# Kernel optimization log

Measured on AMD Instinct MI355X. Metric: run time of the kernel, lower is better.

Reference implementation:

```python
import jax, jax.numpy as jnp
import numpy as np

N, E, F, H, C = 50000, 800000, 128, 128, 64
NEG_SLOPE = 0.2


def setup_inputs() -> dict:
    key = jax.random.key(0)
    ks = jax.random.split(key, 12)
    s = 1.0 / np.sqrt(H)
    return {
        "x": jax.random.normal(ks[0], (N, F), jnp.float32),
        "edge_index": jax.random.randint(ks[1], (2, E), 0, N, jnp.int64),
        "W1": jax.random.normal(ks[2], (F, H), jnp.float32) * s,
        "b1": jnp.zeros((H,), jnp.float32),
        "Wg1": jax.random.normal(ks[3], (H, H), jnp.float32) * s,
        "asrc1": jax.random.normal(ks[4], (H,), jnp.float32) * s,
        "adst1": jax.random.normal(ks[5], (H,), jnp.float32) * s,
        "bg1": jnp.zeros((H,), jnp.float32),
        "W2": jax.random.normal(ks[6], (H, H), jnp.float32) * s,
        "b2": jnp.zeros((H,), jnp.float32),
        "Wg2": jax.random.normal(ks[7], (H, H), jnp.float32) * s,
        "asrc2": jax.random.normal(ks[8], (H,), jnp.float32) * s,
        "adst2": jax.random.normal(ks[9], (H,), jnp.float32) * s,
        "bg2": jnp.zeros((H,), jnp.float32),
        "Wo": jax.random.normal(ks[10], (H, C), jnp.float32) * s,
        "bo": jnp.zeros((C,), jnp.float32),
    }


def _gcn(x, src, dst, n, W, b):
    # PyG GCNConv: add self-loops (done by caller), symmetric normalization
    xw = x @ W
    deg = jax.ops.segment_sum(jnp.ones(src.shape[0], xw.dtype), dst, num_segments=n)
    inv = jax.lax.rsqrt(deg)  # deg >= 1 due to self-loops
    coef = inv[src] * inv[dst]
    return jax.ops.segment_sum(coef[:, None] * xw[src], dst, num_segments=n) + b


def _gat(x, src, dst, n, W, a_s, a_d, b):
    # PyG GATConv, heads=1: segment softmax over destination nodes
    xw = x @ W
    e = jax.nn.leaky_relu((xw @ a_s)[src] + (xw @ a_d)[dst], NEG_SLOPE)
    m = jax.ops.segment_max(e, dst, num_segments=n)
    ex = jnp.exp(e - m[dst])
    denom = jax.ops.segment_sum(ex, dst, num_segments=n)
    alpha = ex / denom[dst]
    return jax.ops.segment_sum(alpha[:, None] * xw[src], dst, num_segments=n) + b


def reference(x, edge_index, W1, b1, Wg1, asrc1, adst1, bg1,
              W2, b2, Wg2, asrc2, adst2, bg2, Wo, bo):
    n = x.shape[0]
    loops = jnp.arange(n, dtype=edge_index.dtype)
    src = jnp.concatenate([edge_index[0], loops])
    dst = jnp.concatenate([edge_index[1], loops])

    h = jax.nn.relu(_gcn(x, src, dst, n, W1, b1))
    h = jax.nn.relu(_gat(h, src, dst, n, Wg1, asrc1, adst1, bg1))
    h = jax.nn.relu(_gcn(h, src, dst, n, W2, b2))
    h = jax.nn.relu(_gat(h, src, dst, n, Wg2, asrc2, adst2, bg2))
    z = h @ Wo + bo
    return (h, z)
```

## Files before the change

kernel.cpp:

```cpp
#include <hip/hip_runtime.h>
#include <hip/hip_bf16.h>
#include <hip/hip_fp16.h>


#define WAVE 64
#define BK 256
#define CHUNK 4096

typedef _Float16 f16x8 __attribute__((ext_vector_type(8)));
typedef float f32x4 __attribute__((ext_vector_type(4)));

__global__ void k_zero_i32(int* __restrict__ p, int n) {
    int i = blockIdx.x * 256 + threadIdx.x;
    if (i < n) p[i] = 0;
}


__global__ __launch_bounds__(256) void k_bhist(
    const int* __restrict__ ei, int* __restrict__ bcnt,
    int E, int Et, int nbuck) {
    __shared__ int hist[256];
    int tid = threadIdx.x;
    if (tid < nbuck) hist[tid] = 0;
    __syncthreads();
    for (int e = blockIdx.x * 256 + tid; e < Et; e += gridDim.x * 256) {
        int d = (e < E) ? ei[E + e] : (e - E);
        atomicAdd(&hist[d >> 8], 1);
    }
    __syncthreads();
    if (tid < nbuck && hist[tid] > 0) atomicAdd(&bcnt[tid], hist[tid]);
}

__global__ void k_bscan(const int* __restrict__ bcnt, int* __restrict__ bbase,
                        int* __restrict__ bcur, int nbuck) {
    __shared__ int tmp[256];
    int tid = threadIdx.x;
    int v = (tid < nbuck) ? bcnt[tid] : 0;
    tmp[tid] = v;
    __syncthreads();
    for (int off = 1; off < 256; off <<= 1) {
        int t = (tid >= off) ? tmp[tid - off] : 0;
        __syncthreads();
        tmp[tid] += t;
        __syncthreads();
    }
    if (tid < nbuck) {
        int excl = tmp[tid] - v;
        bbase[tid] = excl;
        bcur[tid] = excl;
        if (tid == nbuck - 1) bbase[nbuck] = tmp[tid];
    }
}

__global__ __launch_bounds__(256) void k_bscatter(
    const int* __restrict__ ei, int* __restrict__ bcur,
    int2* __restrict__ ebuf, int E, int Et, int nbuck) {
    __shared__ int hist[256];
    __shared__ int base[256];
    __shared__ int off[256];
    constexpr int PT = CHUNK / 256;
    int tid = threadIdx.x;
    int cb = blockIdx.x * CHUNK;
    if (tid < nbuck) { hist[tid] = 0; off[tid] = 0; }
    __syncthreads();

    int sv[PT], dv[PT];
#pragma unroll
    for (int i = 0; i < PT; ++i) {
        int e = cb + i * 256 + tid;
        int s = 0, d = -1;
        if (e < Et) {
            if (e < E) { s = ei[e]; d = ei[E + e]; }
            else       { s = d = e - E; }
            atomicAdd(&hist[d >> 8], 1);
        }
        sv[i] = s; dv[i] = d;
    }
    __syncthreads();
    if (tid < nbuck && hist[tid] > 0)
        base[tid] = atomicAdd(&bcur[tid], hist[tid]);
    __syncthreads();
#pragma unroll
    for (int i = 0; i < PT; ++i) {
        if (dv[i] >= 0) {
            int b = dv[i] >> 8;
            int pos = base[b] + atomicAdd(&off[b], 1);
            ebuf[pos] = make_int2(sv[i], dv[i]);
        }
    }
}

__global__ __launch_bounds__(256) void k_csr(
    const int2* __restrict__ ebuf, const int* __restrict__ bbase,
    int* __restrict__ rowp, float* __restrict__ inv, int* __restrict__ esrc,
    int Nn, int Et) {
    __shared__ int hist[256];
    __shared__ int scan[256];
    __shared__ int cur[256];
    int tid = threadIdx.x;
    int b = blockIdx.x;
    int bb = bbase[b], cnt = bbase[b + 1] - bb;
    hist[tid] = 0;
    __syncthreads();
    for (int t = tid; t < cnt; t += 256)
        atomicAdd(&hist[ebuf[bb + t].y & 255], 1);
    __syncthreads();
    int v = hist[tid];
    scan[tid] = v;
    __syncthreads();
    for (int o = 1; o < 256; o <<= 1) {
        int t = (tid >= o) ? scan[tid - o] : 0;
        __syncthreads();
        scan[tid] += t;
        __syncthreads();
    }
    int excl = scan[tid] - v;
    int node = b * BK + tid;
    if (node < Nn) {
        rowp[node] = bb + excl;
        inv[node] = rsqrtf((float)v);
    }
    cur[tid] = excl;
    if (b == 0 && tid == 0) rowp[Nn] = Et;
    __syncthreads();
    for (int t = tid; t < cnt; t += 256) {
        int2 e = ebuf[bb + t];
        int pos = bb + atomicAdd(&cur[e.y & 255], 1);
        esrc[pos] = e.x;
    }
}


__global__ void k_wcvt(const float* __restrict__ W1, const float* __restrict__ Wg1,
                       const float* __restrict__ W2, const float* __restrict__ Wg2,
                       const float* __restrict__ Wo, __half* __restrict__ Wt) {
    int i = blockIdx.x * 256 + threadIdx.x;
    if (i < 65536) {
        int w = i >> 14;
        int j = i & 16383;
        int nt = j >> 11, ks = (j >> 9) & 3, lane = (j >> 3) & 63, jj = j & 7;
        int n = nt * 16 + (lane & 15);
        int k = ks * 32 + (lane >> 4) * 8 + jj;
        const float* W = (w == 0) ? W1 : (w == 1) ? Wg1 : (w == 2) ? W2 : Wg2;
        Wt[i] = __float2half(W[k * 128 + n]);
    } else if (i < 73728) {
        int j = i - 65536;
        int nt = j >> 11, ks = (j >> 9) & 3, lane = (j >> 3) & 63, jj = j & 7;
        int n = nt * 16 + (lane & 15);
        int k = ks * 32 + (lane >> 4) * 8 + jj;
        Wt[65536 + j] = __float2half(Wo[k * 64 + n]);
    }
}


template <int NC, typename OT>
__global__ __launch_bounds__(256) void gemm_mfma(
    const float* __restrict__ A, const __half* __restrict__ Wt,
    const float* __restrict__ bias, OT* __restrict__ out,
    const float* __restrict__ asrc, const float* __restrict__ adst,
    float* __restrict__ alS, float* __restrict__ alD, int M) {
    constexpr int NT = NC / 16;
    __shared__ f16x8 Wl[NC * 16];
    const int tid = threadIdx.x;
    const int wv = tid >> 6, lane = tid & 63;
    const int m16 = lane & 15, quad = lane >> 4;

#pragma unroll
    for (int i = tid; i < NC * 16; i += 256)
        Wl[i] = ((const f16x8*)Wt)[i];
    __syncthreads();

    const int row0 = blockIdx.x * 64 + wv * 16;

    f16x8 af[4];
    {
        int row = row0 + m16;
        if (row > M - 1) row = M - 1;
        const float* ap = A + (size_t)row * 128 + quad * 8;
#pragma unroll
        for (int ks = 0; ks < 4; ++ks) {
            float4 lo = *(const float4*)(ap + ks * 32);
            float4 hi = *(const float4*)(ap + ks * 32 + 4);
            f16x8 v;
            v[0] = (_Float16)lo.x; v[1] = (_Float16)lo.y;
            v[2] = (_Float16)lo.z; v[3] = (_Float16)lo.w;
            v[4] = (_Float16)hi.x; v[5] = (_Float16)hi.y;
            v[6] = (_Float16)hi.z; v[7] = (_Float16)hi.w;
            af[ks] = v;
        }
    }

    f32x4 acc[NT];
#pragma unroll
    for (int nt = 0; nt < NT; ++nt)
        acc[nt] = (f32x4){0.f, 0.f, 0.f, 0.f};

#pragma unroll
    for (int ks = 0; ks < 4; ++ks) {
#pragma unroll
        for (int nt = 0; nt < NT; ++nt) {
            f16x8 bf = Wl[(nt * 4 + ks) * 64 + lane];
            acc[nt] = __builtin_amdgcn_mfma_f32_16x16x32_f16(
                af[ks], bf, acc[nt], 0, 0, 0);
        }
    }

    if (asrc) {
        float sa[NT], da[NT];
#pragma unroll
        for (int nt = 0; nt < NT; ++nt) {
            sa[nt] = asrc[nt * 16 + m16];
            da[nt] = adst[nt * 16 + m16];
        }
#pragma unroll
        for (int r = 0; r < 4; ++r) {
            float s = 0.f, d = 0.f;
#pragma unroll
            for (int nt = 0; nt < NT; ++nt) {
                s = fmaf(acc[nt][r], sa[nt], s);
                d = fmaf(acc[nt][r], da[nt], d);
            }
#pragma unroll
            for (int off = 8; off > 0; off >>= 1) {
                s += __shfl_xor(s, off);
                d += __shfl_xor(d, off);
            }
            int row = row0 + quad * 4 + r;
            if (m16 == 0 && row < M) { alS[row] = s; alD[row] = d; }
        }
    }

#pragma unroll
    for (int nt = 0; nt < NT; ++nt) {
#pragma unroll
        for (int r = 0; r < 4; ++r) {
            int row = row0 + quad * 4 + r;
            if (row < M) {
                float v = acc[nt][r];
                int col = nt * 16 + m16;
                if constexpr (sizeof(OT) == 2) {
                    ((__half*)out)[(size_t)row * NC + col] = __float2half(v);
                } else {
                    ((float*)out)[(size_t)row * NC + col] = v + bias[col];
                }
            }
        }
    }
}


__device__ __forceinline__ void gather_accum_h(
    const __half* __restrict__ xw, int q, int g, int cnt, int sid, float wgt,
    float acc[8]) {
    for (int base = 0; base < cnt; base += 32) {
        int c = cnt - base;
        float4 x[8];
        float w[8];
#pragma unroll
        for (int u = 0; u < 8; ++u) {
            if (u * 4 < c) {
                int idx = base + 4 * u + g;
                int s = __shfl(sid, idx);
                w[u] = __shfl(wgt, idx);
                x[u] = *(const float4*)(xw + (size_t)s * 128 + q * 8);
            }
        }
#pragma unroll
        for (int u = 0; u < 8; ++u) {
            if (u * 4 < c) {
                const __half2* h2 = (const __half2*)&x[u];
#pragma unroll
                for (int i = 0; i < 4; ++i) {
                    float2 cc = __half22float2(h2[i]);
                    acc[2 * i]     = fmaf(w[u], cc.x, acc[2 * i]);
                    acc[2 * i + 1] = fmaf(w[u], cc.y, acc[2 * i + 1]);
                }
            }
        }
    }
}

__device__ __forceinline__ void finish_store_q(
    float acc[8], const float* __restrict__ bias, float* __restrict__ out,
    int n, int q, int g) {
#pragma unroll
    for (int i = 0; i < 8; ++i) {
        acc[i] += __shfl_xor(acc[i], 16);
        acc[i] += __shfl_xor(acc[i], 32);
    }
    if (g == 0) {
        float4 b0 = ((const float4*)bias)[q * 2];
        float4 b1 = ((const float4*)bias)[q * 2 + 1];
        float4 r0, r1;
        r0.x = fmaxf(acc[0] + b0.x, 0.f);
        r0.y = fmaxf(acc[1] + b0.y, 0.f);
        r0.z = fmaxf(acc[2] + b0.z, 0.f);
        r0.w = fmaxf(acc[3] + b0.w, 0.f);
        r1.x = fmaxf(acc[4] + b1.x, 0.f);
        r1.y = fmaxf(acc[5] + b1.y, 0.f);
        r1.z = fmaxf(acc[6] + b1.z, 0.f);
        r1.w = fmaxf(acc[7] + b1.w, 0.f);
        float4* orow = (float4*)(out + (size_t)n * 128);
        orow[q * 2]     = r0;
        orow[q * 2 + 1] = r1;
    }
}

__global__ __launch_bounds__(256) void k_gcn_agg(
    const __half* __restrict__ xw, const int* __restrict__ rowp,
    const int* __restrict__ esrc, const float* __restrict__ inv,
    const float* __restrict__ bias, float* __restrict__ out, int Nn) {
    int gid = blockIdx.x * 256 + threadIdx.x;
    int n = gid >> 6, lane = gid & 63;
    if (n >= Nn) return;
    int q = lane & 15, g = lane >> 4;
    int beg = rowp[n], end = rowp[n + 1];
    float invd = inv[n];
    float acc[8] = {0.f, 0.f, 0.f, 0.f, 0.f, 0.f, 0.f, 0.f};
    for (int base = beg; base < end; base += WAVE) {
        int e = base + lane;
        bool valid = (e < end);
        int sid = valid ? esrc[e] : 0;
        float c = valid ? invd * inv[sid] : 0.f;
        gather_accum_h(xw, q, g, min(WAVE, end - base), sid, c, acc);
    }
    finish_store_q(acc, bias, out, n, q, g);
}

__global__ __launch_bounds__(256) void k_gat_agg(
    const __half* __restrict__ xw, const int* __restrict__ rowp,
    const int* __restrict__ esrc, const float* __restrict__ as_,
    const float* __restrict__ ad_, const float* __restrict__ bias,
    float* __restrict__ out, int Nn) {
    int gid = blockIdx.x * 256 + threadIdx.x;
    int n = gid >> 6, lane = gid & 63;
    if (n >= Nn) return;
    int q = lane & 15, g = lane >> 4;
    int beg = rowp[n], end = rowp[n + 1];
    int deg = end - beg;
    float adn = ad_[n];
    float acc[8] = {0.f, 0.f, 0.f, 0.f, 0.f, 0.f, 0.f, 0.f};

    if (deg <= WAVE) {
        bool valid = (lane < deg);
        int sid = 0;
        float v = -1e30f;
        if (valid) {
            sid = esrc[beg + lane];
            float t = as_[sid] + adn;
            v = (t > 0.f) ? t : 0.2f * t;
        }
        float m = v;
#pragma unroll
        for (int off = 32; off > 0; off >>= 1) m = fmaxf(m, __shfl_xor(m, off));
        float ex = valid ? __expf(v - m) : 0.f;
        float ssum = ex;
#pragma unroll
        for (int off = 32; off > 0; off >>= 1) ssum += __shfl_xor(ssum, off);
        float wgt = ex * (1.f / ssum);
        gather_accum_h(xw, q, g, deg, sid, wgt, acc);
    } else {
        float m = -1e30f, ssum = 0.f;
        for (int e = beg + lane; e < end; e += WAVE) {
            float v = as_[esrc[e]] + adn;
            v = (v > 0.f) ? v : 0.2f * v;
            float mn = fmaxf(m, v);
            ssum = ssum * __expf(m - mn) + __expf(v - mn);
            m = mn;
        }
#pragma unroll
        for (int off = 32; off > 0; off >>= 1) {
            float mo = __shfl_xor(m, off);
            float so = __shfl_xor(ssum, off);
            float mn = fmaxf(m, mo);
            ssum = ssum * __expf(m - mn) + so * __expf(mo - mn);
            m = mn;
        }
        float rden = 1.f / ssum;
        for (int base = beg; base < end; base += WAVE) {
            int e = base + lane;
            bool valid = (e < end);
            int sid = valid ? esrc[e] : 0;
            float wgt = 0.f;
            if (valid) {
                float v = as_[sid] + adn;
                v = (v > 0.f) ? v : 0.2f * v;
                wgt = __expf(v - m) * rden;
            }
            gather_accum_h(xw, q, g, min(WAVE, end - base), sid, wgt, acc);
        }
    }
    finish_store_q(acc, bias, out, n, q, g);
}


extern "C" void kernel_launch(void* const* d_in, const int* in_sizes, int n_in,
                              void* d_out, int out_size, void* d_ws, size_t ws_size,
                              hipStream_t stream) {
    const float* x   = (const float*)d_in[0];
    const int*   ei  = (const int*)d_in[1];
    const float* W1  = (const float*)d_in[2];
    const float* b1  = (const float*)d_in[3];
    const float* Wg1 = (const float*)d_in[4];
    const float* as1 = (const float*)d_in[5];
    const float* ad1 = (const float*)d_in[6];
    const float* bg1 = (const float*)d_in[7];
    const float* W2  = (const float*)d_in[8];
    const float* b2  = (const float*)d_in[9];
    const float* Wg2 = (const float*)d_in[10];
    const float* as2 = (const float*)d_in[11];
    const float* ad2 = (const float*)d_in[12];
    const float* bg2 = (const float*)d_in[13];
    const float* Wo  = (const float*)d_in[14];
    const float* bo  = (const float*)d_in[15];

    const int Nn = in_sizes[0] / 128;
    const int E  = in_sizes[1] / 2;
    const int Et = E + Nn;
    const int H  = 128;
    const int nbuck = (Nn + BK - 1) / BK;

    float* outH = (float*)d_out;
    float* outZ = outH + (size_t)Nn * H;

    char* p = (char*)d_ws;
    auto carve = [&](size_t bytes) {
        char* r = p;
        p += (bytes + 255) & ~(size_t)255;
        return r;
    };
    __half* bufA = (__half*)carve((size_t)Nn * H * sizeof(__half));
    __half* Wt   = (__half*)carve((size_t)73728 * sizeof(__half));
    float* alS   = (float*)carve((size_t)Nn * sizeof(float));
    float* alD   = (float*)carve((size_t)Nn * sizeof(float));
    float* inv   = (float*)carve((size_t)Nn * sizeof(float));
    int*   rowp  = (int*)carve((size_t)(Nn + 1) * sizeof(int));
    int*   esrc  = (int*)carve((size_t)Et * sizeof(int));
    int2*  ebuf  = (int2*)carve((size_t)Et * sizeof(int2));
    int*   bcnt  = (int*)carve((size_t)nbuck * sizeof(int));
    int*   bbase = (int*)carve((size_t)(nbuck + 1) * sizeof(int));
    int*   bcur  = (int*)carve((size_t)nbuck * sizeof(int));
    (void)ws_size; (void)n_in; (void)out_size;

    const int aggBlocks = (Nn * WAVE + 255) / 256;
    const int gemmB = (Nn + 63) / 64;
    const int scatB = (Et + CHUNK - 1) / CHUNK;

    k_zero_i32<<<1, 256, 0, stream>>>(bcnt, nbuck);
    k_bhist<<<104, 256, 0, stream>>>(ei, bcnt, E, Et, nbuck);
    k_bscan<<<1, 256, 0, stream>>>(bcnt, bbase, bcur, nbuck);
    k_bscatter<<<scatB, 256, 0, stream>>>(ei, bcur, ebuf, E, Et, nbuck);
    k_csr<<<nbuck, 256, 0, stream>>>(ebuf, bbase, rowp, inv, esrc, Nn, Et);
    k_wcvt<<<288, 256, 0, stream>>>(W1, Wg1, W2, Wg2, Wo, Wt);

    gemm_mfma<128, __half><<<gemmB, 256, 0, stream>>>(
        x, Wt, nullptr, bufA, nullptr, nullptr, nullptr, nullptr, Nn);
    k_gcn_agg<<<aggBlocks, 256, 0, stream>>>(bufA, rowp, esrc, inv, b1, outH, Nn);

    gemm_mfma<128, __half><<<gemmB, 256, 0, stream>>>(
        outH, Wt + 16384, nullptr, bufA, as1, ad1, alS, alD, Nn);
    k_gat_agg<<<aggBlocks, 256, 0, stream>>>(bufA, rowp, esrc, alS, alD, bg1, outH, Nn);

    gemm_mfma<128, __half><<<gemmB, 256, 0, stream>>>(
        outH, Wt + 32768, nullptr, bufA, nullptr, nullptr, nullptr, nullptr, Nn);
    k_gcn_agg<<<aggBlocks, 256, 0, stream>>>(bufA, rowp, esrc, inv, b2, outH, Nn);

    gemm_mfma<128, __half><<<gemmB, 256, 0, stream>>>(
        outH, Wt + 49152, nullptr, bufA, as2, ad2, alS, alD, Nn);
    k_gat_agg<<<aggBlocks, 256, 0, stream>>>(bufA, rowp, esrc, alS, alD, bg2, outH, Nn);

    gemm_mfma<64, float><<<gemmB, 256, 0, stream>>>(
        outH, Wt + 65536, bo, outZ, nullptr, nullptr, nullptr, nullptr, Nn);
}
```

Before: 378.4 us.

## Slice feature layout and precompute per-edge weights for sliced aggregation

```diff
diff --git a/kernel.cpp b/kernel.cpp
--- a/kernel.cpp
+++ b/kernel.cpp
@@ -6,6 +6,7 @@
 #define WAVE 64
 #define BK 256
 #define CHUNK 4096
+#define NSLICE 4
 
 typedef _Float16 f16x8 __attribute__((ext_vector_type(8)));
 typedef float f32x4 __attribute__((ext_vector_type(4)));
@@ -239,7 +240,8 @@
                 float v = acc[nt][r];
                 int col = nt * 16 + m16;
                 if constexpr (sizeof(OT) == 2) {
-                    ((__half*)out)[(size_t)row * NC + col] = __float2half(v);
+                    size_t addr = ((size_t)(col >> 5) * M + row) * 32 + (col & 31);
+                    ((__half*)out)[addr] = __float2half(v);
                 } else {
                     ((float*)out)[(size_t)row * NC + col] = v + bias[col];
                 }
@@ -249,97 +251,30 @@
 }
 
 
-__device__ __forceinline__ void gather_accum_h(
-    const __half* __restrict__ xw, int q, int g, int cnt, int sid, float wgt,
-    float acc[8]) {
-    for (int base = 0; base < cnt; base += 32) {
-        int c = cnt - base;
-        float4 x[8];
-        float w[8];
-#pragma unroll
-        for (int u = 0; u < 8; ++u) {
-            if (u * 4 < c) {
-                int idx = base + 4 * u + g;
-                int s = __shfl(sid, idx);
-                w[u] = __shfl(wgt, idx);
-                x[u] = *(const float4*)(xw + (size_t)s * 128 + q * 8);
-            }
-        }
-#pragma unroll
-        for (int u = 0; u < 8; ++u) {
-            if (u * 4 < c) {
-                const __half2* h2 = (const __half2*)&x[u];
-#pragma unroll
-                for (int i = 0; i < 4; ++i) {
-                    float2 cc = __half22float2(h2[i]);
-                    acc[2 * i]     = fmaf(w[u], cc.x, acc[2 * i]);
-                    acc[2 * i + 1] = fmaf(w[u], cc.y, acc[2 * i + 1]);
-                }
-            }
-        }
-    }
-}
-
-__device__ __forceinline__ void finish_store_q(
-    float acc[8], const float* __restrict__ bias, float* __restrict__ out,
-    int n, int q, int g) {
-#pragma unroll
-    for (int i = 0; i < 8; ++i) {
-        acc[i] += __shfl_xor(acc[i], 16);
-        acc[i] += __shfl_xor(acc[i], 32);
-    }
-    if (g == 0) {
-        float4 b0 = ((const float4*)bias)[q * 2];
-        float4 b1 = ((const float4*)bias)[q * 2 + 1];
-        float4 r0, r1;
-        r0.x = fmaxf(acc[0] + b0.x, 0.f);
-        r0.y = fmaxf(acc[1] + b0.y, 0.f);
-        r0.z = fmaxf(acc[2] + b0.z, 0.f);
-        r0.w = fmaxf(acc[3] + b0.w, 0.f);
-        r1.x = fmaxf(acc[4] + b1.x, 0.f);
-        r1.y = fmaxf(acc[5] + b1.y, 0.f);
-        r1.z = fmaxf(acc[6] + b1.z, 0.f);
-        r1.w = fmaxf(acc[7] + b1.w, 0.f);
-        float4* orow = (float4*)(out + (size_t)n * 128);
-        orow[q * 2]     = r0;
-        orow[q * 2 + 1] = r1;
-    }
-}
-
-__global__ __launch_bounds__(256) void k_gcn_agg(
-    const __half* __restrict__ xw, const int* __restrict__ rowp,
-    const int* __restrict__ esrc, const float* __restrict__ inv,
-    const float* __restrict__ bias, float* __restrict__ out, int Nn) {
+__global__ __launch_bounds__(256) void k_wgcn(
+    const int* __restrict__ rowp, const int* __restrict__ esrc,
+    const float* __restrict__ inv, int2* __restrict__ ew, int Nn) {
     int gid = blockIdx.x * 256 + threadIdx.x;
     int n = gid >> 6, lane = gid & 63;
     if (n >= Nn) return;
-    int q = lane & 15, g = lane >> 4;
     int beg = rowp[n], end = rowp[n + 1];
     float invd = inv[n];
-    float acc[8] = {0.f, 0.f, 0.f, 0.f, 0.f, 0.f, 0.f, 0.f};
-    for (int base = beg; base < end; base += WAVE) {
-        int e = base + lane;
-        bool valid = (e < end);
-        int sid = valid ? esrc[e] : 0;
-        float c = valid ? invd * inv[sid] : 0.f;
-        gather_accum_h(xw, q, g, min(WAVE, end - base), sid, c, acc);
-    }
-    finish_store_q(acc, bias, out, n, q, g);
-}
-
-__global__ __launch_bounds__(256) void k_gat_agg(
-    const __half* __restrict__ xw, const int* __restrict__ rowp,
-    const int* __restrict__ esrc, const float* __restrict__ as_,
-    const float* __restrict__ ad_, const float* __restrict__ bias,
-    float* __restrict__ out, int Nn) {
+    for (int e = beg + lane; e < end; e += WAVE) {
+        int sid = esrc[e];
+        ew[e] = make_int2(sid, __float_as_int(invd * inv[sid]));
+    }
+}
+
+__global__ __launch_bounds__(256) void k_alpha(
+    const int* __restrict__ rowp, const int* __restrict__ esrc,
+    const float* __restrict__ as_, const float* __restrict__ ad_,
+    int2* __restrict__ ew, int Nn) {
     int gid = blockIdx.x * 256 + threadIdx.x;
     int n = gid >> 6, lane = gid & 63;
     if (n >= Nn) return;
-    int q = lane & 15, g = lane >> 4;
     int beg = rowp[n], end = rowp[n + 1];
     int deg = end - beg;
     float adn = ad_[n];
-    float acc[8] = {0.f, 0.f, 0.f, 0.f, 0.f, 0.f, 0.f, 0.f};
 
     if (deg <= WAVE) {
         bool valid = (lane < deg);
@@ -358,7 +293,7 @@
 #pragma unroll
         for (int off = 32; off > 0; off >>= 1) ssum += __shfl_xor(ssum, off);
         float wgt = ex * (1.f / ssum);
-        gather_accum_h(xw, q, g, deg, sid, wgt, acc);
+        if (valid) ew[beg + lane] = make_int2(sid, __float_as_int(wgt));
     } else {
         float m = -1e30f, ssum = 0.f;
         for (int e = beg + lane; e < end; e += WAVE) {
@@ -377,20 +312,74 @@
             m = mn;
         }
         float rden = 1.f / ssum;
-        for (int base = beg; base < end; base += WAVE) {
-            int e = base + lane;
-            bool valid = (e < end);
-            int sid = valid ? esrc[e] : 0;
-            float wgt = 0.f;
-            if (valid) {
-                float v = as_[sid] + adn;
-                v = (v > 0.f) ? v : 0.2f * v;
-                wgt = __expf(v - m) * rden;
-            }
-            gather_accum_h(xw, q, g, min(WAVE, end - base), sid, wgt, acc);
-        }
-    }
-    finish_store_q(acc, bias, out, n, q, g);
+        for (int e = beg + lane; e < end; e += WAVE) {
+            int sid = esrc[e];
+            float v = as_[sid] + adn;
+            v = (v > 0.f) ? v : 0.2f * v;
+            ew[e] = make_int2(sid, __float_as_int(__expf(v - m) * rden));
+        }
+    }
+}
+
+
+__device__ __forceinline__ void acc8(float acc[8], float4 v, float w) {
+    const __half2* h2 = (const __half2*)&v;
+#pragma unroll
+    for (int i = 0; i < 4; ++i) {
+        float2 f = __half22float2(h2[i]);
+        acc[2 * i]     = fmaf(w, f.x, acc[2 * i]);
+        acc[2 * i + 1] = fmaf(w, f.y, acc[2 * i + 1]);
+    }
+}
+
+__global__ __launch_bounds__(256) void k_agg(
+    const __half* __restrict__ xw2, const int* __restrict__ rowp,
+    const int2* __restrict__ ew, const float* __restrict__ bias,
+    float* __restrict__ out, int Nn) {
+    int tid = threadIdx.x;
+    int slice = blockIdx.x & 3;
+    int nb = blockIdx.x >> 2;
+    int wv = tid >> 6, lane = tid & 63;
+    int n = nb * 64 + wv * 16 + (lane >> 2);
+    int q = lane & 3;
+    if (n >= Nn) return;
+    int beg = rowp[n], end = rowp[n + 1];
+    const __half* xs = xw2 + (size_t)slice * Nn * 32 + q * 8;
+
+    float acc[8] = {0.f, 0.f, 0.f, 0.f, 0.f, 0.f, 0.f, 0.f};
+    int e = beg;
+    for (; e + 4 <= end; e += 4) {
+        int2 p0 = ew[e], p1 = ew[e + 1], p2 = ew[e + 2], p3 = ew[e + 3];
+        float4 v0 = *(const float4*)(xs + (size_t)p0.x * 32);
+        float4 v1 = *(const float4*)(xs + (size_t)p1.x * 32);
+        float4 v2 = *(const float4*)(xs + (size_t)p2.x * 32);
+        float4 v3 = *(const float4*)(xs + (size_t)p3.x * 32);
+        acc8(acc, v0, __int_as_float(p0.y));
+        acc8(acc, v1, __int_as_float(p1.y));
+        acc8(acc, v2, __int_as_float(p2.y));
+        acc8(acc, v3, __int_as_float(p3.y));
+    }
+    for (; e < end; ++e) {
+        int2 p = ew[e];
+        float4 v = *(const float4*)(xs + (size_t)p.x * 32);
+        acc8(acc, v, __int_as_float(p.y));
+    }
+
+    const float* bp = bias + slice * 32 + q * 8;
+    float4 b0 = *(const float4*)(bp);
+    float4 b1 = *(const float4*)(bp + 4);
+    float4 r0, r1;
+    r0.x = fmaxf(acc[0] + b0.x, 0.f);
+    r0.y = fmaxf(acc[1] + b0.y, 0.f);
+    r0.z = fmaxf(acc[2] + b0.z, 0.f);
+    r0.w = fmaxf(acc[3] + b0.w, 0.f);
+    r1.x = fmaxf(acc[4] + b1.x, 0.f);
+    r1.y = fmaxf(acc[5] + b1.y, 0.f);
+    r1.z = fmaxf(acc[6] + b1.z, 0.f);
+    r1.w = fmaxf(acc[7] + b1.w, 0.f);
+    float4* o = (float4*)(out + (size_t)n * 128 + slice * 32 + q * 8);
+    o[0] = r0;
+    o[1] = r1;
 }
 
 
@@ -437,13 +426,17 @@
     int*   rowp  = (int*)carve((size_t)(Nn + 1) * sizeof(int));
     int*   esrc  = (int*)carve((size_t)Et * sizeof(int));
     int2*  ebuf  = (int2*)carve((size_t)Et * sizeof(int2));
+    int2*  ewg   = (int2*)carve((size_t)Et * sizeof(int2));
     int*   bcnt  = (int*)carve((size_t)nbuck * sizeof(int));
     int*   bbase = (int*)carve((size_t)(nbuck + 1) * sizeof(int));
     int*   bcur  = (int*)carve((size_t)nbuck * sizeof(int));
     (void)ws_size; (void)n_in; (void)out_size;
 
-    const int aggBlocks = (Nn * WAVE + 255) / 256;
+    int2* ewa = ebuf;
+
+    const int nodeWaves = (Nn * WAVE + 255) / 256;
     const int gemmB = (Nn + 63) / 64;
+    const int aggB  = ((Nn + 63) / 64) * NSLICE;
     const int scatB = (Et + CHUNK - 1) / CHUNK;
 
     k_zero_i32<<<1, 256, 0, stream>>>(bcnt, nbuck);
@@ -452,22 +445,25 @@
     k_bscatter<<<scatB, 256, 0, stream>>>(ei, bcur, ebuf, E, Et, nbuck);
     k_csr<<<nbuck, 256, 0, stream>>>(ebuf, bbase, rowp, inv, esrc, Nn, Et);
     k_wcvt<<<288, 256, 0, stream>>>(W1, Wg1, W2, Wg2, Wo, Wt);
+    k_wgcn<<<nodeWaves, 256, 0, stream>>>(rowp, esrc, inv, ewg, Nn);
 
     gemm_mfma<128, __half><<<gemmB, 256, 0, stream>>>(
         x, Wt, nullptr, bufA, nullptr, nullptr, nullptr, nullptr, Nn);
-    k_gcn_agg<<<aggBlocks, 256, 0, stream>>>(bufA, rowp, esrc, inv, b1, outH, Nn);
+    k_agg<<<aggB, 256, 0, stream>>>(bufA, rowp, ewg, b1, outH, Nn);
 
     gemm_mfma<128, __half><<<gemmB, 256, 0, stream>>>(
         outH, Wt + 16384, nullptr, bufA, as1, ad1, alS, alD, Nn);
-    k_gat_agg<<<aggBlocks, 256, 0, stream>>>(bufA, rowp, esrc, alS, alD, bg1, outH, Nn);
+    k_alpha<<<nodeWaves, 256, 0, stream>>>(rowp, esrc, alS, alD, ewa, Nn);
+    k_agg<<<aggB, 256, 0, stream>>>(bufA, rowp, ewa, bg1, outH, Nn);
 
     gemm_mfma<128, __half><<<gemmB, 256, 0, stream>>>(
         outH, Wt + 32768, nullptr, bufA, nullptr, nullptr, nullptr, nullptr, Nn);
-    k_gcn_agg<<<aggBlocks, 256, 0, stream>>>(bufA, rowp, esrc, inv, b2, outH, Nn);
+    k_agg<<<aggB, 256, 0, stream>>>(bufA, rowp, ewg, b2, outH, Nn);
 
     gemm_mfma<128, __half><<<gemmB, 256, 0, stream>>>(
         outH, Wt + 49152, nullptr, bufA, as2, ad2, alS, alD, Nn);
-    k_gat_agg<<<aggBlocks, 256, 0, stream>>>(bufA, rowp, esrc, alS, alD, bg2, outH, Nn);
+    k_alpha<<<nodeWaves, 256, 0, stream>>>(rowp, esrc, alS, alD, ewa, Nn);
+    k_agg<<<aggB, 256, 0, stream>>>(bufA, rowp, ewa, bg2, outH, Nn);
 
     gemm_mfma<64, float><<<gemmB, 256, 0, stream>>>(
         outH, Wt + 65536, bo, outZ, nullptr, nullptr, nullptr, nullptr, Nn);
```

After: 382.0 us. Within noise of the previous version (+1.0%).

## Sort CSR neighbors and precompute packed edge weights for unified aggregation

Applied to the files above, without the earlier changes.

```diff
diff --git a/kernel.cpp b/kernel.cpp
--- a/kernel.cpp
+++ b/kernel.cpp
@@ -127,6 +127,50 @@
         int2 e = ebuf[bb + t];
         int pos = bb + atomicAdd(&cur[e.y & 255], 1);
         esrc[pos] = e.x;
+    }
+}
+
+
+__global__ __launch_bounds__(256) void k_sortw(
+    const int* __restrict__ rowp, int* __restrict__ esrc,
+    const float* __restrict__ inv, int2* __restrict__ ewg, int Nn) {
+    int gid = blockIdx.x * 256 + threadIdx.x;
+    int n = gid >> 6, lane = gid & 63;
+    if (n >= Nn) return;
+    int beg = rowp[n], end = rowp[n + 1];
+    int deg = end - beg;
+    float invn = inv[n];
+
+    if (deg <= WAVE) {
+        int key = (lane < deg) ? esrc[beg + lane] : 0x7fffffff;
+#pragma unroll
+        for (int k = 2; k <= 64; k <<= 1) {
+#pragma unroll
+            for (int j = k >> 1; j >= 1; j >>= 1) {
+                int pk = __shfl_xor(key, j);
+                bool up = ((lane & k) == 0);
+                bool lower = ((lane & j) == 0);
+                int mn = min(key, pk), mx = max(key, pk);
+                key = (lower == up) ? mn : mx;
+            }
+        }
+        if (lane < deg) {
+            esrc[beg + lane] = key;
+            ewg[beg + lane] = make_int2(key, __float_as_int(invn * inv[key]));
+        }
+    } else {
+        if (lane == 0) {
+            for (int i = beg + 1; i < end; ++i) {
+                int v = esrc[i];
+                int j = i - 1;
+                while (j >= beg && esrc[j] > v) { esrc[j + 1] = esrc[j]; --j; }
+                esrc[j + 1] = v;
+            }
+            for (int i = beg; i < end; ++i) {
+                int s = esrc[i];
+                ewg[i] = make_int2(s, __float_as_int(invn * inv[s]));
+            }
+        }
     }
 }
 
@@ -249,6 +293,63 @@
 }
 
 
+__global__ __launch_bounds__(256) void k_alpha(
+    const int* __restrict__ rowp, const int* __restrict__ esrc,
+    const float* __restrict__ as_, const float* __restrict__ ad_,
+    int2* __restrict__ ew, int Nn) {
+    int gid = blockIdx.x * 256 + threadIdx.x;
+    int n = gid >> 6, lane = gid & 63;
+    if (n >= Nn) return;
+    int beg = rowp[n], end = rowp[n + 1];
+    int deg = end - beg;
+    float adn = ad_[n];
+
+    if (deg <= WAVE) {
+        bool valid = (lane < deg);
+        int sid = 0;
+        float v = -1e30f;
+        if (valid) {
+            sid = esrc[beg + lane];
+            float t = as_[sid] + adn;
+            v = (t > 0.f) ? t : 0.2f * t;
+        }
+        float m = v;
+#pragma unroll
+        for (int off = 32; off > 0; off >>= 1) m = fmaxf(m, __shfl_xor(m, off));
+        float ex = valid ? __expf(v - m) : 0.f;
+        float ssum = ex;
+#pragma unroll
+        for (int off = 32; off > 0; off >>= 1) ssum += __shfl_xor(ssum, off);
+        float wgt = ex * (1.f / ssum);
+        if (valid) ew[beg + lane] = make_int2(sid, __float_as_int(wgt));
+    } else {
+        float m = -1e30f, ssum = 0.f;
+        for (int e = beg + lane; e < end; e += WAVE) {
+            float v = as_[esrc[e]] + adn;
+            v = (v > 0.f) ? v : 0.2f * v;
+            float mn = fmaxf(m, v);
+            ssum = ssum * __expf(m - mn) + __expf(v - mn);
+            m = mn;
+        }
+#pragma unroll
+        for (int off = 32; off > 0; off >>= 1) {
+            float mo = __shfl_xor(m, off);
+            float so = __shfl_xor(ssum, off);
+            float mn = fmaxf(m, mo);
+            ssum = ssum * __expf(m - mn) + so * __expf(mo - mn);
+            m = mn;
+        }
+        float rden = 1.f / ssum;
+        for (int e = beg + lane; e < end; e += WAVE) {
+            int sid = esrc[e];
+            float v = as_[sid] + adn;
+            v = (v > 0.f) ? v : 0.2f * v;
+            ew[e] = make_int2(sid, __float_as_int(__expf(v - m) * rden));
+        }
+    }
+}
+
+
 __device__ __forceinline__ void gather_accum_h(
     const __half* __restrict__ xw, int q, int g, int cnt, int sid, float wgt,
     float acc[8]) {
@@ -306,89 +407,22 @@
     }
 }
 
-__global__ __launch_bounds__(256) void k_gcn_agg(
+__global__ __launch_bounds__(256) void k_agg(
     const __half* __restrict__ xw, const int* __restrict__ rowp,
-    const int* __restrict__ esrc, const float* __restrict__ inv,
-    const float* __restrict__ bias, float* __restrict__ out, int Nn) {
-    int gid = blockIdx.x * 256 + threadIdx.x;
-    int n = gid >> 6, lane = gid & 63;
-    if (n >= Nn) return;
-    int q = lane & 15, g = lane >> 4;
-    int beg = rowp[n], end = rowp[n + 1];
-    float invd = inv[n];
-    float acc[8] = {0.f, 0.f, 0.f, 0.f, 0.f, 0.f, 0.f, 0.f};
-    for (int base = beg; base < end; base += WAVE) {
-        int e = base + lane;
-        bool valid = (e < end);
-        int sid = valid ? esrc[e] : 0;
-        float c = valid ? invd * inv[sid] : 0.f;
-        gather_accum_h(xw, q, g, min(WAVE, end - base), sid, c, acc);
-    }
-    finish_store_q(acc, bias, out, n, q, g);
-}
-
-__global__ __launch_bounds__(256) void k_gat_agg(
-    const __half* __restrict__ xw, const int* __restrict__ rowp,
-    const int* __restrict__ esrc, const float* __restrict__ as_,
-    const float* __restrict__ ad_, const float* __restrict__ bias,
+    const int2* __restrict__ ew, const float* __restrict__ bias,
     float* __restrict__ out, int Nn) {
     int gid = blockIdx.x * 256 + threadIdx.x;
     int n = gid >> 6, lane = gid & 63;
     if (n >= Nn) return;
     int q = lane & 15, g = lane >> 4;
     int beg = rowp[n], end = rowp[n + 1];
-    int deg = end - beg;
-    float adn = ad_[n];
     float acc[8] = {0.f, 0.f, 0.f, 0.f, 0.f, 0.f, 0.f, 0.f};
-
-    if (deg <= WAVE) {
-        bool valid = (lane < deg);
-        int sid = 0;
-        float v = -1e30f;
-        if (valid) {
-            sid = esrc[beg + lane];
-            float t = as_[sid] + adn;
-            v = (t > 0.f) ? t : 0.2f * t;
-        }
-        float m = v;
-#pragma unroll
-        for (int off = 32; off > 0; off >>= 1) m = fmaxf(m, __shfl_xor(m, off));
-        float ex = valid ? __expf(v - m) : 0.f;
-        float ssum = ex;
-#pragma unroll
-        for (int off = 32; off > 0; off >>= 1) ssum += __shfl_xor(ssum, off);
-        float wgt = ex * (1.f / ssum);
-        gather_accum_h(xw, q, g, deg, sid, wgt, acc);
-    } else {
-        float m = -1e30f, ssum = 0.f;
-        for (int e = beg + lane; e < end; e += WAVE) {
-            float v = as_[esrc[e]] + adn;
-            v = (v > 0.f) ? v : 0.2f * v;
-            float mn = fmaxf(m, v);
-            ssum = ssum * __expf(m - mn) + __expf(v - mn);
-            m = mn;
-        }
-#pragma unroll
-        for (int off = 32; off > 0; off >>= 1) {
-            float mo = __shfl_xor(m, off);
-            float so = __shfl_xor(ssum, off);
-            float mn = fmaxf(m, mo);
-            ssum = ssum * __expf(m - mn) + so * __expf(mo - mn);
-            m = mn;
-        }
-        float rden = 1.f / ssum;
-        for (int base = beg; base < end; base += WAVE) {
-            int e = base + lane;
-            bool valid = (e < end);
-            int sid = valid ? esrc[e] : 0;
-            float wgt = 0.f;
-            if (valid) {
-                float v = as_[sid] + adn;
-                v = (v > 0.f) ? v : 0.2f * v;
-                wgt = __expf(v - m) * rden;
-            }
-            gather_accum_h(xw, q, g, min(WAVE, end - base), sid, wgt, acc);
-        }
+    for (int base = beg; base < end; base += WAVE) {
+        int e = base + lane;
+        bool valid = (e < end);
+        int2 p = valid ? ew[e] : make_int2(0, 0);
+        gather_accum_h(xw, q, g, min(WAVE, end - base), p.x,
+                       __int_as_float(p.y), acc);
     }
     finish_store_q(acc, bias, out, n, q, g);
 }
@@ -437,12 +471,15 @@
     int*   rowp  = (int*)carve((size_t)(Nn + 1) * sizeof(int));
     int*   esrc  = (int*)carve((size_t)Et * sizeof(int));
     int2*  ebuf  = (int2*)carve((size_t)Et * sizeof(int2));
+    int2*  ewg   = (int2*)carve((size_t)Et * sizeof(int2));
     int*   bcnt  = (int*)carve((size_t)nbuck * sizeof(int));
     int*   bbase = (int*)carve((size_t)(nbuck + 1) * sizeof(int));
     int*   bcur  = (int*)carve((size_t)nbuck * sizeof(int));
     (void)ws_size; (void)n_in; (void)out_size;
 
-    const int aggBlocks = (Nn * WAVE + 255) / 256;
+    int2* ewa = ebuf;
+
+    const int nodeWaves = (Nn * WAVE + 255) / 256;
     const int gemmB = (Nn + 63) / 64;
     const int scatB = (Et + CHUNK - 1) / CHUNK;
 
@@ -452,22 +489,25 @@
     k_bscatter<<<scatB, 256, 0, stream>>>(ei, bcur, ebuf, E, Et, nbuck);
     k_csr<<<nbuck, 256, 0, stream>>>(ebuf, bbase, rowp, inv, esrc, Nn, Et);
     k_wcvt<<<288, 256, 0, stream>>>(W1, Wg1, W2, Wg2, Wo, Wt);
+    k_sortw<<<nodeWaves, 256, 0, stream>>>(rowp, esrc, inv, ewg, Nn);
 
     gemm_mfma<128, __half><<<gemmB, 256, 0, stream>>>(
         x, Wt, nullptr, bufA, nullptr, nullptr, nullptr, nullptr, Nn);
-    k_gcn_agg<<<aggBlocks, 256, 0, stream>>>(bufA, rowp, esrc, inv, b1, outH, Nn);
+    k_agg<<<nodeWaves, 256, 0, stream>>>(bufA, rowp, ewg, b1, outH, Nn);
 
     gemm_mfma<128, __half><<<gemmB, 256, 0, stream>>>(
         outH, Wt + 16384, nullptr, bufA, as1, ad1, alS, alD, Nn);
-    k_gat_agg<<<aggBlocks, 256, 0, stream>>>(bufA, rowp, esrc, alS, alD, bg1, outH, Nn);
+    k_alpha<<<nodeWaves, 256, 0, stream>>>(rowp, esrc, alS, alD, ewa, Nn);
+    k_agg<<<nodeWaves, 256, 0, stream>>>(bufA, rowp, ewa, bg1, outH, Nn);
 
     gemm_mfma<128, __half><<<gemmB, 256, 0, stream>>>(
         outH, Wt + 32768, nullptr, bufA, nullptr, nullptr, nullptr, nullptr, Nn);
-    k_gcn_agg<<<aggBlocks, 256, 0, stream>>>(bufA, rowp, esrc, inv, b2, outH, Nn);
+    k_agg<<<nodeWaves, 256, 0, stream>>>(bufA, rowp, ewg, b2, outH, Nn);
 
     gemm_mfma<128, __half><<<gemmB, 256, 0, stream>>>(
         outH, Wt + 49152, nullptr, bufA, as2, ad2, alS, alD, Nn);
-    k_gat_agg<<<aggBlocks, 256, 0, stream>>>(bufA, rowp, esrc, alS, alD, bg2, outH, Nn);
+    k_alpha<<<nodeWaves, 256, 0, stream>>>(rowp, esrc, alS, alD, ewa, Nn);
+    k_agg<<<nodeWaves, 256, 0, stream>>>(bufA, rowp, ewa, bg2, outH, Nn);
 
     gemm_mfma<64, float><<<gemmB, 256, 0, stream>>>(
         outH, Wt + 65536, bo, outZ, nullptr, nullptr, nullptr, nullptr, Nn);
```

Result: slower. 400.9 us (+6.0%).

## Fuse GEMM and aggregation layers into one cooperative persistent kernel

Applied to the files above, without the earlier changes.

```diff
diff --git a/kernel.cpp b/kernel.cpp
--- a/kernel.cpp
+++ b/kernel.cpp
@@ -1,7 +1,10 @@
 #include <hip/hip_runtime.h>
+#include <hip/hip_cooperative_groups.h>
 #include <hip/hip_bf16.h>
 #include <hip/hip_fp16.h>
 
+
+namespace cg = cooperative_groups;
 
 #define WAVE 64
 #define BK 256
@@ -154,100 +157,95 @@
 
 
 template <int NC, typename OT>
-__global__ __launch_bounds__(256) void gemm_mfma(
-    const float* __restrict__ A, const __half* __restrict__ Wt,
+__device__ __forceinline__ void gemm_phase(
+    const float* __restrict__ A, const __half* __restrict__ Wtp,
     const float* __restrict__ bias, OT* __restrict__ out,
     const float* __restrict__ asrc, const float* __restrict__ adst,
-    float* __restrict__ alS, float* __restrict__ alD, int M) {
+    float* __restrict__ alS, float* __restrict__ alD,
+    int M, int wgid, int gwaves, int lane) {
     constexpr int NT = NC / 16;
-    __shared__ f16x8 Wl[NC * 16];
-    const int tid = threadIdx.x;
-    const int wv = tid >> 6, lane = tid & 63;
     const int m16 = lane & 15, quad = lane >> 4;
-
-#pragma unroll
-    for (int i = tid; i < NC * 16; i += 256)
-        Wl[i] = ((const f16x8*)Wt)[i];
-    __syncthreads();
-
-    const int row0 = blockIdx.x * 64 + wv * 16;
-
-    f16x8 af[4];
-    {
-        int row = row0 + m16;
-        if (row > M - 1) row = M - 1;
-        const float* ap = A + (size_t)row * 128 + quad * 8;
+    const f16x8* Wf = (const f16x8*)Wtp;
+    const int tiles = (M + 15) >> 4;
+
+    for (int t = wgid; t < tiles; t += gwaves) {
+        const int row0 = t * 16;
+        f16x8 af[4];
+        {
+            int row = row0 + m16;
+            if (row > M - 1) row = M - 1;
+            const float* ap = A + (size_t)row * 128 + quad * 8;
+#pragma unroll
+            for (int ks = 0; ks < 4; ++ks) {
+                float4 lo = *(const float4*)(ap + ks * 32);
+                float4 hi = *(const float4*)(ap + ks * 32 + 4);
+                f16x8 v;
+                v[0] = (_Float16)lo.x; v[1] = (_Float16)lo.y;
+                v[2] = (_Float16)lo.z; v[3] = (_Float16)lo.w;
+                v[4] = (_Float16)hi.x; v[5] = (_Float16)hi.y;
+                v[6] = (_Float16)hi.z; v[7] = (_Float16)hi.w;
+                af[ks] = v;
+            }
+        }
+
+        f32x4 acc[NT];
+#pragma unroll
+        for (int nt = 0; nt < NT; ++nt)
+            acc[nt] = (f32x4){0.f, 0.f, 0.f, 0.f};
+
 #pragma unroll
         for (int ks = 0; ks < 4; ++ks) {
-            float4 lo = *(const float4*)(ap + ks * 32);
-            float4 hi = *(const float4*)(ap + ks * 32 + 4);
-            f16x8 v;
-            v[0] = (_Float16)lo.x; v[1] = (_Float16)lo.y;
-            v[2] = (_Float16)lo.z; v[3] = (_Float16)lo.w;
-            v[4] = (_Float16)hi.x; v[5] = (_Float16)hi.y;
-            v[6] = (_Float16)hi.z; v[7] = (_Float16)hi.w;
-            af[ks] = v;
-        }
-    }
-
-    f32x4 acc[NT];
-#pragma unroll
-    for (int nt = 0; nt < NT; ++nt)
-        acc[nt] = (f32x4){0.f, 0.f, 0.f, 0.f};
-
-#pragma unroll
-    for (int ks = 0; ks < 4; ++ks) {
+#pragma unroll
+            for (int nt = 0; nt < NT; ++nt) {
+                f16x8 bf = Wf[(nt * 4 + ks) * 64 + lane];
+                acc[nt] = __builtin_amdgcn_mfma_f32_16x16x32_f16(
+                    af[ks], bf, acc[nt], 0, 0, 0);
+            }
+        }
+
+        if (asrc) {
+            float sa[NT], da[NT];
+#pragma unroll
+            for (int nt = 0; nt < NT; ++nt) {
+                sa[nt] = asrc[nt * 16 + m16];
+                da[nt] = adst[nt * 16 + m16];
+            }
+#pragma unroll
+            for (int r = 0; r < 4; ++r) {
+                float s = 0.f, d = 0.f;
+#pragma unroll
+                for (int nt = 0; nt < NT; ++nt) {
+                    s = fmaf(acc[nt][r], sa[nt], s);
+                    d = fmaf(acc[nt][r], da[nt], d);
+                }
+#pragma unroll
+                for (int off = 8; off > 0; off >>= 1) {
+                    s += __shfl_xor(s, off);
+                    d += __shfl_xor(d, off);
+                }
+                int row = row0 + quad * 4 + r;
+                if (m16 == 0 && row < M) { alS[row] = s; alD[row] = d; }
+            }
+        }
+
 #pragma unroll
         for (int nt = 0; nt < NT; ++nt) {
-            f16x8 bf = Wl[(nt * 4 + ks) * 64 + lane];
-            acc[nt] = __builtin_amdgcn_mfma_f32_16x16x32_f16(
-                af[ks], bf, acc[nt], 0, 0, 0);
-        }
-    }
-
-    if (asrc) {
-        float sa[NT], da[NT];
-#pragma unroll
-        for (int nt = 0; nt < NT; ++nt) {
-            sa[nt] = asrc[nt * 16 + m16];
-            da[nt] = adst[nt * 16 + m16];
-        }
-#pragma unroll
-        for (int r = 0; r < 4; ++r) {
-            float s = 0.f, d = 0.f;
-#pragma unroll
-            for (int nt = 0; nt < NT; ++nt) {
-                s = fmaf(acc[nt][r], sa[nt], s);
-                d = fmaf(acc[nt][r], da[nt], d);
-            }
-#pragma unroll
-            for (int off = 8; off > 0; off >>= 1) {
-                s += __shfl_xor(s, off);
-                d += __shfl_xor(d, off);
-            }
-            int row = row0 + quad * 4 + r;
-            if (m16 == 0 && row < M) { alS[row] = s; alD[row] = d; }
-        }
-    }
-
-#pragma unroll
-    for (int nt = 0; nt < NT; ++nt) {
-#pragma unroll
-        for (int r = 0; r < 4; ++r) {
-            int row = row0 + quad * 4 + r;
-            if (row < M) {
-                float v = acc[nt][r];
-                int col = nt * 16 + m16;
-                if constexpr (sizeof(OT) == 2) {
-                    ((__half*)out)[(size_t)row * NC + col] = __float2half(v);
-                } else {
-                    ((float*)out)[(size_t)row * NC + col] = v + bias[col];
+#pragma unroll
+            for (int r = 0; r < 4; ++r) {
+                int row = row0 + quad * 4 + r;
+                if (row < M) {
+                    float v = acc[nt][r];
+                    int col = nt * 16 + m16;
+                    if constexpr (sizeof(OT) == 2) {
+                        ((__half*)out)[(size_t)row * NC + col] = __float2half(v);
+                    } else {
+                        ((float*)out)[(size_t)row * NC + col] = v + bias[col];
+                    }
                 }
             }
         }
     }
 }
-
 
 __device__ __forceinline__ void gather_accum_h(
     const __half* __restrict__ xw, int q, int g, int cnt, int sid, float wgt,
@@ -306,91 +304,155 @@
     }
 }
 
-__global__ __launch_bounds__(256) void k_gcn_agg(
+__device__ __forceinline__ void gcn_phase(
     const __half* __restrict__ xw, const int* __restrict__ rowp,
     const int* __restrict__ esrc, const float* __restrict__ inv,
-    const float* __restrict__ bias, float* __restrict__ out, int Nn) {
-    int gid = blockIdx.x * 256 + threadIdx.x;
-    int n = gid >> 6, lane = gid & 63;
-    if (n >= Nn) return;
-    int q = lane & 15, g = lane >> 4;
-    int beg = rowp[n], end = rowp[n + 1];
-    float invd = inv[n];
-    float acc[8] = {0.f, 0.f, 0.f, 0.f, 0.f, 0.f, 0.f, 0.f};
-    for (int base = beg; base < end; base += WAVE) {
-        int e = base + lane;
-        bool valid = (e < end);
-        int sid = valid ? esrc[e] : 0;
-        float c = valid ? invd * inv[sid] : 0.f;
-        gather_accum_h(xw, q, g, min(WAVE, end - base), sid, c, acc);
-    }
-    finish_store_q(acc, bias, out, n, q, g);
-}
-
-__global__ __launch_bounds__(256) void k_gat_agg(
-    const __half* __restrict__ xw, const int* __restrict__ rowp,
-    const int* __restrict__ esrc, const float* __restrict__ as_,
-    const float* __restrict__ ad_, const float* __restrict__ bias,
-    float* __restrict__ out, int Nn) {
-    int gid = blockIdx.x * 256 + threadIdx.x;
-    int n = gid >> 6, lane = gid & 63;
-    if (n >= Nn) return;
-    int q = lane & 15, g = lane >> 4;
-    int beg = rowp[n], end = rowp[n + 1];
-    int deg = end - beg;
-    float adn = ad_[n];
-    float acc[8] = {0.f, 0.f, 0.f, 0.f, 0.f, 0.f, 0.f, 0.f};
-
-    if (deg <= WAVE) {
-        bool valid = (lane < deg);
-        int sid = 0;
-        float v = -1e30f;
-        if (valid) {
-            sid = esrc[beg + lane];
-            float t = as_[sid] + adn;
-            v = (t > 0.f) ? t : 0.2f * t;
-        }
-        float m = v;
-#pragma unroll
-        for (int off = 32; off > 0; off >>= 1) m = fmaxf(m, __shfl_xor(m, off));
-        float ex = valid ? __expf(v - m) : 0.f;
-        float ssum = ex;
-#pragma unroll
-        for (int off = 32; off > 0; off >>= 1) ssum += __shfl_xor(ssum, off);
-        float wgt = ex * (1.f / ssum);
-        gather_accum_h(xw, q, g, deg, sid, wgt, acc);
-    } else {
-        float m = -1e30f, ssum = 0.f;
-        for (int e = beg + lane; e < end; e += WAVE) {
-            float v = as_[esrc[e]] + adn;
-            v = (v > 0.f) ? v : 0.2f * v;
-            float mn = fmaxf(m, v);
-            ssum = ssum * __expf(m - mn) + __expf(v - mn);
-            m = mn;
-        }
-#pragma unroll
-        for (int off = 32; off > 0; off >>= 1) {
-            float mo = __shfl_xor(m, off);
-            float so = __shfl_xor(ssum, off);
-            float mn = fmaxf(m, mo);
-            ssum = ssum * __expf(m - mn) + so * __expf(mo - mn);
-            m = mn;
-        }
-        float rden = 1.f / ssum;
+    const float* __restrict__ bias, float* __restrict__ out,
+    int Nn, int wgid, int gwaves, int lane) {
+    const int q = lane & 15, g = lane >> 4;
+    for (int n = wgid; n < Nn; n += gwaves) {
+        int beg = rowp[n], end = rowp[n + 1];
+        float invd = inv[n];
+        float acc[8] = {0.f, 0.f, 0.f, 0.f, 0.f, 0.f, 0.f, 0.f};
         for (int base = beg; base < end; base += WAVE) {
             int e = base + lane;
             bool valid = (e < end);
             int sid = valid ? esrc[e] : 0;
-            float wgt = 0.f;
+            float c = valid ? invd * inv[sid] : 0.f;
+            gather_accum_h(xw, q, g, min(WAVE, end - base), sid, c, acc);
+        }
+        finish_store_q(acc, bias, out, n, q, g);
+    }
+}
+
+__device__ __forceinline__ void gat_phase(
+    const __half* __restrict__ xw, const int* __restrict__ rowp,
+    const int* __restrict__ esrc, const float* __restrict__ as_,
+    const float* __restrict__ ad_, const float* __restrict__ bias,
+    float* __restrict__ out, int Nn, int wgid, int gwaves, int lane) {
+    const int q = lane & 15, g = lane >> 4;
+    for (int n = wgid; n < Nn; n += gwaves) {
+        int beg = rowp[n], end = rowp[n + 1];
+        int deg = end - beg;
+        float adn = ad_[n];
+        float acc[8] = {0.f, 0.f, 0.f, 0.f, 0.f, 0.f, 0.f, 0.f};
+
+        if (deg <= WAVE) {
+            bool valid = (lane < deg);
+            int sid = 0;
+            float v = -1e30f;
             if (valid) {
-                float v = as_[sid] + adn;
+                sid = esrc[beg + lane];
+                float t = as_[sid] + adn;
+                v = (t > 0.f) ? t : 0.2f * t;
+            }
+            float m = v;
+#pragma unroll
+            for (int off = 32; off > 0; off >>= 1) m = fmaxf(m, __shfl_xor(m, off));
+            float ex = valid ? __expf(v - m) : 0.f;
+            float ssum = ex;
+#pragma unroll
+            for (int off = 32; off > 0; off >>= 1) ssum += __shfl_xor(ssum, off);
+            float wgt = ex * (1.f / ssum);
+            gather_accum_h(xw, q, g, deg, sid, wgt, acc);
+        } else {
+            float m = -1e30f, ssum = 0.f;
+            for (int e = beg + lane; e < end; e += WAVE) {
+                float v = as_[esrc[e]] + adn;
                 v = (v > 0.f) ? v : 0.2f * v;
-                wgt = __expf(v - m) * rden;
-            }
-            gather_accum_h(xw, q, g, min(WAVE, end - base), sid, wgt, acc);
-        }
-    }
-    finish_store_q(acc, bias, out, n, q, g);
+                float mn = fmaxf(m, v);
+                ssum = ssum * __expf(m - mn) + __expf(v - mn);
+                m = mn;
+            }
+#pragma unroll
+            for (int off = 32; off > 0; off >>= 1) {
+                float mo = __shfl_xor(m, off);
+                float so = __shfl_xor(ssum, off);
+                float mn = fmaxf(m, mo);
+                ssum = ssum * __expf(m - mn) + so * __expf(mo - mn);
+                m = mn;
+            }
+            float rden = 1.f / ssum;
+            for (int base = beg; base < end; base += WAVE) {
+                int e = base + lane;
+                bool valid = (e < end);
+                int sid = valid ? esrc[e] : 0;
+                float wgt = 0.f;
+                if (valid) {
+                    float v = as_[sid] + adn;
+                    v = (v > 0.f) ? v : 0.2f * v;
+                    wgt = __expf(v - m) * rden;
+                }
+                gather_accum_h(xw, q, g, min(WAVE, end - base), sid, wgt, acc);
+            }
+        }
+        finish_store_q(acc, bias, out, n, q, g);
+    }
+}
+
+
+struct MegaArgs {
+    const float* x;
+    const __half* Wt;
+    const int* rowp;
+    const int* esrc;
+    const float* inv;
+    const float *b1, *as1, *ad1, *bg1;
+    const float *b2, *as2, *ad2, *bg2;
+    const float* bo;
+    __half* bufA;
+    float *alS, *alD;
+    float* outH;
+    float* outZ;
+    int Nn;
+};
+
+__device__ __forceinline__ void run_phase(const MegaArgs& a, int ph,
+                                          int wgid, int gwaves, int lane) {
+    switch (ph) {
+    case 0: gemm_phase<128, __half>(a.x, a.Wt, nullptr, a.bufA,
+                nullptr, nullptr, nullptr, nullptr, a.Nn, wgid, gwaves, lane); break;
+    case 1: gcn_phase(a.bufA, a.rowp, a.esrc, a.inv, a.b1, a.outH,
+                a.Nn, wgid, gwaves, lane); break;
+    case 2: gemm_phase<128, __half>(a.outH, a.Wt + 16384, nullptr, a.bufA,
+                a.as1, a.ad1, a.alS, a.alD, a.Nn, wgid, gwaves, lane); break;
+    case 3: gat_phase(a.bufA, a.rowp, a.esrc, a.alS, a.alD, a.bg1, a.outH,
+                a.Nn, wgid, gwaves, lane); break;
+    case 4: gemm_phase<128, __half>(a.outH, a.Wt + 32768, nullptr, a.bufA,
+                nullptr, nullptr, nullptr, nullptr, a.Nn, wgid, gwaves, lane); break;
+    case 5: gcn_phase(a.bufA, a.rowp, a.esrc, a.inv, a.b2, a.outH,
+                a.Nn, wgid, gwaves, lane); break;
+    case 6: gemm_phase<128, __half>(a.outH, a.Wt + 49152, nullptr, a.bufA,
+                a.as2, a.ad2, a.alS, a.alD, a.Nn, wgid, gwaves, lane); break;
+    case 7: gat_phase(a.bufA, a.rowp, a.esrc, a.alS, a.alD, a.bg2, a.outH,
+                a.Nn, wgid, gwaves, lane); break;
+    case 8: gemm_phase<64, float>(a.outH, a.Wt + 65536, a.bo, a.outZ,
+                nullptr, nullptr, nullptr, nullptr, a.Nn, wgid, gwaves, lane); break;
+    }
+}
+
+__global__ __launch_bounds__(256, 4) void k_mega(MegaArgs a) {
+    cg::grid_group grid = cg::this_grid();
+    const int lane = threadIdx.x & 63;
+    const int wgid = blockIdx.x * 4 + (threadIdx.x >> 6);
+    const int gwaves = gridDim.x * 4;
+
+    run_phase(a, 0, wgid, gwaves, lane); grid.sync();
+    run_phase(a, 1, wgid, gwaves, lane); grid.sync();
+    run_phase(a, 2, wgid, gwaves, lane); grid.sync();
+    run_phase(a, 3, wgid, gwaves, lane); grid.sync();
+    run_phase(a, 4, wgid, gwaves, lane); grid.sync();
+    run_phase(a, 5, wgid, gwaves, lane); grid.sync();
+    run_phase(a, 6, wgid, gwaves, lane); grid.sync();
+    run_phase(a, 7, wgid, gwaves, lane); grid.sync();
+    run_phase(a, 8, wgid, gwaves, lane);
+}
+
+__global__ __launch_bounds__(256, 4) void k_phase(MegaArgs a, int ph) {
+    const int lane = threadIdx.x & 63;
+    const int wgid = blockIdx.x * 4 + (threadIdx.x >> 6);
+    const int gwaves = gridDim.x * 4;
+    run_phase(a, ph, wgid, gwaves, lane);
 }
 
 
@@ -442,8 +504,6 @@
     int*   bcur  = (int*)carve((size_t)nbuck * sizeof(int));
     (void)ws_size; (void)n_in; (void)out_size;
 
-    const int aggBlocks = (Nn * WAVE + 255) / 256;
-    const int gemmB = (Nn + 63) / 64;
     const int scatB = (Et + CHUNK - 1) / CHUNK;
 
     k_zero_i32<<<1, 256, 0, stream>>>(bcnt, nbuck);
@@ -453,22 +513,31 @@
     k_csr<<<nbuck, 256, 0, stream>>>(ebuf, bbase, rowp, inv, esrc, Nn, Et);
     k_wcvt<<<288, 256, 0, stream>>>(W1, Wg1, W2, Wg2, Wo, Wt);
 
-    gemm_mfma<128, __half><<<gemmB, 256, 0, stream>>>(
-        x, Wt, nullptr, bufA, nullptr, nullptr, nullptr, nullptr, Nn);
-    k_gcn_agg<<<aggBlocks, 256, 0, stream>>>(bufA, rowp, esrc, inv, b1, outH, Nn);
-
-    gemm_mfma<128, __half><<<gemmB, 256, 0, stream>>>(
-        outH, Wt + 16384, nullptr, bufA, as1, ad1, alS, alD, Nn);
-    k_gat_agg<<<aggBlocks, 256, 0, stream>>>(bufA, rowp, esrc, alS, alD, bg1, outH, Nn);
-
-    gemm_mfma<128, __half><<<gemmB, 256, 0, stream>>>(
-        outH, Wt + 32768, nullptr, bufA, nullptr, nullptr, nullptr, nullptr, Nn);
-    k_gcn_agg<<<aggBlocks, 256, 0, stream>>>(bufA, rowp, esrc, inv, b2, outH, Nn);
-
-    gemm_mfma<128, __half><<<gemmB, 256, 0, stream>>>(
-        outH, Wt + 49152, nullptr, bufA, as2, ad2, alS, alD, Nn);
-    k_gat_agg<<<aggBlocks, 256, 0, stream>>>(bufA, rowp, esrc, alS, alD, bg2, outH, Nn);
-
-    gemm_mfma<64, float><<<gemmB, 256, 0, stream>>>(
-        outH, Wt + 65536, bo, outZ, nullptr, nullptr, nullptr, nullptr, Nn);
-}
+    MegaArgs ma;
+    ma.x = x; ma.Wt = Wt; ma.rowp = rowp; ma.esrc = esrc; ma.inv = inv;
+    ma.b1 = b1; ma.as1 = as1; ma.ad1 = ad1; ma.bg1 = bg1;
+    ma.b2 = b2; ma.as2 = as2; ma.ad2 = ad2; ma.bg2 = bg2;
+    ma.bo = bo; ma.bufA = bufA; ma.alS = alS; ma.alD = alD;
+    ma.outH = outH; ma.outZ = outZ; ma.Nn = Nn;
+
+    static int coopBpc = -2;
+    if (coopBpc == -2) {
+        int bpc = 0;
+        if (hipOccupancyMaxActiveBlocksPerMultiprocessor(&bpc, k_mega, 256, 0)
+            != hipSuccess) bpc = 0;
+        coopBpc = bpc;
+    }
+
+    bool done = false;
+    if (coopBpc >= 2) {
+        int G = (coopBpc >= 4 ? 4 : coopBpc) * 256;
+        void* ka[] = { (void*)&ma };
+        if (hipLaunchCooperativeKernel(k_mega, dim3(G), dim3(256), ka, 0, stream)
+            == hipSuccess) done = true;
+        else coopBpc = 0;
+    }
+    if (!done) {
+        for (int ph = 0; ph < 9; ++ph)
+            k_phase<<<1024, 256, 0, stream>>>(ma, ph);
+    }
+}
```

Measured after the change: 1.091 ms. 188% more time.
